# Optimization experiments

Measured on AMD Instinct MI355X. Metric: run time of the kernel, lower is better.

## Reference

```python
import jax, jax.numpy as jnp
import numpy as np

N, E, B, A = 102400, 1638400, 256, 7


def setup_inputs() -> dict:
    key = jax.random.key(0)
    ks = jax.random.split(key, 24)
    rn = lambda k, s, sc=0.1: jax.random.normal(k, s, jnp.float32) * sc
    return {
        "x": jax.random.normal(ks[0], (N, 5), jnp.float32),
        "edge_index": jax.random.randint(ks[1], (2, E), 0, N, jnp.int32),
        "edge_attr": jax.random.normal(ks[2], (E, 1), jnp.float32),
        "agent_state": jax.random.normal(ks[3], (B, 34), jnp.float32),
        "pool_batch": jnp.sort(jax.random.randint(ks[4], (N,), 0, B, jnp.int32)),
        # GATConv params (heads=1, concat): lin [5,64], lin_edge [1,64], att vectors [64], bias [64]
        "W_gat": rn(ks[5], (5, 64)), "att_src": rn(ks[6], (64,)), "att_dst": rn(ks[7], (64,)),
        "W_edge": rn(ks[8], (1, 64)), "att_edge": rn(ks[9], (64,)), "b_gat": rn(ks[10], (64,)),
        "W_fc1": rn(ks[11], (64, 128)), "b_fc1": rn(ks[12], (128,)),
        "W_fc2": rn(ks[13], (34, 64)), "b_fc2": rn(ks[14], (64,)),
        "W_v1": rn(ks[15], (192, 128)), "b_v1": rn(ks[16], (128,)),
        "W_v2": rn(ks[17], (128, 1)), "b_v2": rn(ks[18], (1,)),
        "W_a1": rn(ks[19], (192, 128)), "b_a1": rn(ks[20], (128,)),
        "W_a2": rn(ks[21], (128, A)), "b_a2": rn(ks[22], (A,)),
    }


def _gat(x, edge_index, edge_attr, W_gat, att_src, att_dst, W_edge, att_edge, b_gat):
    n = x.shape[0]
    # add self-loops (PyG default), self-loop edge_attr = mean of edge_attr
    loop = jnp.arange(n, dtype=edge_index.dtype)
    src = jnp.concatenate([edge_index[0], loop])
    dst = jnp.concatenate([edge_index[1], loop])
    ea = jnp.concatenate([edge_attr, jnp.broadcast_to(edge_attr.mean(0), (n, edge_attr.shape[1]))], 0)
    h = x @ W_gat                                  # [N,64]
    a_s = h @ att_src                              # [N]
    a_d = h @ att_dst                              # [N]
    a_e = (ea @ W_edge) @ att_edge                 # [E+N]
    alpha = jax.nn.leaky_relu(a_s[src] + a_d[dst] + a_e, 0.2)
    # segment softmax over incoming edges per destination node
    m = jax.ops.segment_max(alpha, dst, num_segments=n)
    ex = jnp.exp(alpha - m[dst])
    s = jax.ops.segment_sum(ex, dst, num_segments=n)
    w = ex / (s[dst] + 1e-16)
    out = jax.ops.segment_sum(w[:, None] * h[src], dst, num_segments=n)
    return out + b_gat


def reference(x, edge_index, edge_attr, agent_state, pool_batch,
              W_gat, att_src, att_dst, W_edge, att_edge, b_gat,
              W_fc1, b_fc1, W_fc2, b_fc2,
              W_v1, b_v1, W_v2, b_v2, W_a1, b_a1, W_a2, b_a2):
    h = _gat(x, edge_index, edge_attr, W_gat, att_src, att_dst, W_edge, att_edge, b_gat)
    h = jax.nn.relu(h @ W_fc1 + b_fc1)             # [N,128]
    # global mean pool over graphs
    ssum = jax.ops.segment_sum(h, pool_batch, num_segments=B)
    cnt = jax.ops.segment_sum(jnp.ones((h.shape[0],), h.dtype), pool_batch, num_segments=B)
    g = ssum / jnp.maximum(cnt, 1.0)[:, None]      # [B,128]
    a = jax.nn.relu(agent_state @ W_fc2 + b_fc2)   # [B,64]
    z = jnp.concatenate([g, a], -1)                # [B,192]
    value = jax.nn.relu(z @ W_v1 + b_v1) @ W_v2 + b_v2
    adv = jax.nn.relu(z @ W_a1 + b_a1) @ W_a2 + b_a2
    return value + adv - adv.mean(-1, keepdims=True)
```

## Files before the change

kernel.cpp:

```cpp
#include <hip/hip_runtime.h>
#include <hip/hip_fp16.h>
#include <math.h>

#define NPB   512
#define NPBL  9
#define HSTR  5
#define MAXR  256
#define TILE  2048
#define RPT   8
#define GCS   16
#define SLICES 8

static __device__ __forceinline__ float lrelu(float x) { return x > 0.0f ? x : 0.2f * x; }

static __device__ __forceinline__ unsigned pk2(float a, float b) {
    __half2 h = __floats2half2_rn(a, b);
    return *reinterpret_cast<unsigned*>(&h);
}
static __device__ __forceinline__ float2 up2(unsigned u) {
    __half2 h = *reinterpret_cast<__half2*>(&u);
    return __half22float2(h);
}


__global__ void k_setup(const float* __restrict__ W_gat, const float* __restrict__ att_src,
                        const float* __restrict__ att_dst, const float* __restrict__ W_edge,
                        const float* __restrict__ att_edge, const float* __restrict__ b_gat,
                        const float* __restrict__ W_fc1, const float* __restrict__ b_fc1,
                        float* __restrict__ consts, unsigned* __restrict__ gcur,
                        float* __restrict__ epart8) {
    int t = threadIdx.x;
    for (int i = t; i < MAXR * GCS; i += 128) gcur[i] = 0u;
    if (t < 8) epart8[t] = 0.f;
    if (t == 0) {
        float c = 0.f;
        for (int k = 0; k < 64; k++) c += W_edge[k] * att_edge[k];
        consts[1] = c;
    }
    if (t < 5) {
        float a = 0.f, b = 0.f;
        for (int c = 0; c < 64; c++) {
            float w = W_gat[t * 64 + c];
            a += w * att_src[c];
            b += w * att_dst[c];
        }
        consts[2 + t] = a;
        consts[7 + t] = b;
    }
    float bcv = b_fc1[t];
    for (int c = 0; c < 64; c++) bcv += b_gat[c] * W_fc1[c * 128 + t];
    consts[16 + t] = bcv;
    for (int k = 0; k < 5; k++) {
        float w = 0.f;
        for (int c = 0; c < 64; c++) w += W_gat[k * 64 + c] * W_fc1[c * 128 + t];
        consts[144 + k * 128 + t] = w;
    }
}

__global__ void k_np1(const float* __restrict__ x, const float* __restrict__ consts,
                      uint4* __restrict__ xh, float* __restrict__ a_s, float* __restrict__ a_d,
                      const int* __restrict__ pb, int* __restrict__ bstart,
                      const int* __restrict__ src, const int* __restrict__ dst,
                      const float* __restrict__ ea,
                      uint2* __restrict__ slab, unsigned* __restrict__ gcur,
                      float* __restrict__ epart8,
                      int N, int B, int E, int R, int CAP, int nbl) {
    if ((int)blockIdx.x < nbl) {
        int i = blockIdx.x * blockDim.x + threadIdx.x;
        if (i >= N) return;
        const float* xi = x + (size_t)i * 5;
        float x0 = xi[0], x1 = xi[1], x2 = xi[2], x3 = xi[3], x4 = xi[4];
        float as = x0 * consts[2] + x1 * consts[3] + x2 * consts[4] + x3 * consts[5] + x4 * consts[6];
        float ad = x0 * consts[7] + x1 * consts[8] + x2 * consts[9] + x3 * consts[10] + x4 * consts[11];
        uint4 pkv;
        pkv.x = pk2(x0, x1);
        pkv.y = pk2(x2, x3);
        pkv.z = pk2(x4, 1.0f);
        pkv.w = __float_as_uint(as);
        xh[i] = pkv;
        a_s[i] = as;
        a_d[i] = ad;
        int cur = pb[i];
        int prev = (i == 0) ? -1 : pb[i - 1];
        for (int b = prev + 1; b <= cur; b++) bstart[b] = i;
        if (i == N - 1)
            for (int b = cur + 1; b <= B; b++) bstart[b] = N;
        return;
    }
    __shared__ unsigned hist[MAXR], lbase[MAXR], gbase[MAXR], scan[256];
    __shared__ uint2 staged[TILE];
    __shared__ unsigned char bof[TILE];
    __shared__ float esum[256];
    int t = threadIdx.x;
    int e0 = ((int)blockIdx.x - nbl) * TILE;
    int n = E - e0; if (n > TILE) n = TILE;
    for (int i = t; i < MAXR; i += 256) hist[i] = 0;
    __syncthreads();
    unsigned key[RPT]; float val[RPT]; unsigned brk[RPT];
    float ce = consts[1];
    float easc = 0.f;
#pragma unroll
    for (int k = 0; k < RPT; k++) {
        int idx = t + k * 256;
        brk[k] = 0xFFFFFFFFu;
        if (idx < n) {
            int e = e0 + idx;
            int d = dst[e];
            unsigned b = (unsigned)d >> NPBL;
            key[k] = ((unsigned)src[e] << NPBL) | ((unsigned)d & (NPB - 1));
            float eav = ea[e];
            easc += eav;
            val[k] = ce * eav;
            unsigned r = atomicAdd(&hist[b], 1u);
            brk[k] = (b << 12) | r;
        }
    }
    __syncthreads();
    unsigned v = (t < R) ? hist[t] : 0;
    if (t < R) gbase[t] = atomicAdd(&gcur[t * GCS], v);
    scan[t] = v;
    __syncthreads();
    for (int off = 1; off < 256; off <<= 1) {
        unsigned add = (t >= off) ? scan[t - off] : 0;
        __syncthreads();
        scan[t] += add;
        __syncthreads();
    }
    if (t < R) lbase[t] = scan[t] - v;
    __syncthreads();
#pragma unroll
    for (int k = 0; k < RPT; k++) {
        if (brk[k] != 0xFFFFFFFFu) {
            unsigned b = brk[k] >> 12, r = brk[k] & 4095u;
            unsigned pos = lbase[b] + r;
            staged[pos] = make_uint2(key[k], __float_as_uint(val[k]));
            bof[pos] = (unsigned char)b;
        }
    }
    __syncthreads();
    for (int i = t; i < n; i += 256) {
        unsigned b = bof[i];
        unsigned slot = gbase[b] + (unsigned)i - lbase[b];
        if (slot < (unsigned)CAP) slab[(size_t)b * CAP + slot] = staged[i];
    }
    esum[t] = easc;
    __syncthreads();
    for (int o = 128; o > 0; o >>= 1) {
        if (t < o) esum[t] += esum[t + o];
        __syncthreads();
    }
    if (t == 0) unsafeAtomicAdd(&epart8[blockIdx.x & 7], esum[0]);
}

__global__ void k_p2(const uint2* __restrict__ slab, const unsigned* __restrict__ gcur,
                     const uint4* __restrict__ xh, const float* __restrict__ a_d,
                     unsigned* __restrict__ partials, const float* __restrict__ epart8,
                     float* __restrict__ consts_w, int S, int CAP, int N) {
    __shared__ __half2 accH[NPB * HSTR];
    __shared__ float adl[NPB];
    int t = threadIdx.x;
    int s = blockIdx.x, r = blockIdx.y;
    if (s == 0 && r == 0 && t == 0) {
        float se = 0.f;
        for (int i = 0; i < 8; i++) se += epart8[i];
        consts_w[0] = se;
    }
    for (int i = t; i < NPB; i += 256) {
        int node = r * NPB + i;
        adl[i] = (node < N) ? a_d[node] : 0.f;
    }
    __half2 z2 = __floats2half2_rn(0.f, 0.f);
    for (int i = t; i < NPB * HSTR; i += 256) accH[i] = z2;
    __syncthreads();
    unsigned cnt = gcur[r * GCS]; if (cnt > (unsigned)CAP) cnt = CAP;
    unsigned L = (cnt + (unsigned)S - 1) / (unsigned)S;
    unsigned i0 = (unsigned)s * L, i1 = i0 + L; if (i1 > cnt) i1 = cnt;
    const uint2* sl = slab + (size_t)r * CAP;
    for (unsigned i = i0 + t; i < i1; i += 256) {
        uint2 rec = sl[i];
        uint4 v = xh[rec.x >> NPBL];
        unsigned dl = rec.x & (NPB - 1);
        float al = __uint_as_float(v.w) + adl[dl] + __uint_as_float(rec.y);
        float ex = __expf(lrelu(al));
        __half2 ex2 = __half2half2(__float2half(ex));
        __half2* a = accH + dl * HSTR;
        unsafeAtomicAdd(a + 0, __hmul2(ex2, *reinterpret_cast<const __half2*>(&v.x)));
        unsafeAtomicAdd(a + 1, __hmul2(ex2, *reinterpret_cast<const __half2*>(&v.y)));
        unsafeAtomicAdd(a + 2, __hmul2(ex2, *reinterpret_cast<const __half2*>(&v.z)));
    }
    __syncthreads();
    unsigned* out = partials + (size_t)(r * S + s) * (NPB * 3);
    for (int j = t; j < NPB * 3; j += 256) {
        int comp = j >> NPBL, dl = j & (NPB - 1);
        out[j] = *reinterpret_cast<unsigned*>(&accH[dl * HSTR + comp]);
    }
}

__global__ void k_p3(const unsigned* __restrict__ partials, const float* __restrict__ x,
                     const float* __restrict__ a_s, const float* __restrict__ a_d,
                     const float* __restrict__ consts, float* __restrict__ y,
                     int N, int S, float inv_E) {
    int i = blockIdx.x * blockDim.x + threadIdx.x;
    if (i >= N) return;
    int r = i >> NPBL, dl = i & (NPB - 1);
    float2 y01 = make_float2(0.f, 0.f), y23 = make_float2(0.f, 0.f), y4s = make_float2(0.f, 0.f);
    const unsigned* p = partials + (size_t)r * S * (NPB * 3) + dl;
    for (int s = 0; s < S; s++) {
        const unsigned* q = p + (size_t)s * (NPB * 3);
        float2 a = up2(q[0 * NPB]), b = up2(q[1 * NPB]), c = up2(q[2 * NPB]);
        y01.x += a.x; y01.y += a.y;
        y23.x += b.x; y23.y += b.y;
        y4s.x += c.x; y4s.y += c.y;
    }
    const float* xi = x + (size_t)i * 5;
    float x0 = xi[0], x1 = xi[1], x2 = xi[2], x3 = xi[3], x4 = xi[4];
    float mean_ea = consts[0] * inv_E;
    float aself = lrelu(a_s[i] + a_d[i] + consts[1] * mean_ea);
    float exs = __expf(aself);
    float inv = 1.f / (y4s.y + exs + 1e-16f);
    y[0 * (size_t)N + i] = (y01.x + exs * x0) * inv;
    y[1 * (size_t)N + i] = (y01.y + exs * x1) * inv;
    y[2 * (size_t)N + i] = (y23.x + exs * x2) * inv;
    y[3 * (size_t)N + i] = (y23.y + exs * x3) * inv;
    y[4 * (size_t)N + i] = (y4s.x + exs * x4) * inv;
}

__global__ void k_pool(const float* __restrict__ y, const float* __restrict__ consts,
                       const int* __restrict__ bstart, float* __restrict__ g4, int B, int N) {
    int l = threadIdx.x;
    int b = blockIdx.x >> 2, q = blockIdx.x & 3;
    int st = bstart[b], en = bstart[b + 1];
    int len = en - st;
    int qlen = (len + 3) >> 2;
    int i0 = st + q * qlen;
    int i1 = i0 + qlen;
    if (i0 > en) i0 = en;
    if (i1 > en) i1 = en;
    float w0 = consts[144 + l], w1 = consts[272 + l], w2 = consts[400 + l],
          w3 = consts[528 + l], w4 = consts[656 + l];
    float bc = consts[16 + l];
    const float* y0 = y;
    const float* y1p = y + (size_t)N;
    const float* y2p = y + 2 * (size_t)N;
    const float* y3p = y + 3 * (size_t)N;
    const float* y4p = y + 4 * (size_t)N;
    float a0 = 0.f, a1 = 0.f, a2 = 0.f, a3 = 0.f;
    int i = i0;
    for (; i + 3 < i1; i += 4) {
        float h0 = bc + y0[i] * w0 + y1p[i] * w1 + y2p[i] * w2 + y3p[i] * w3 + y4p[i] * w4;
        float h1 = bc + y0[i+1] * w0 + y1p[i+1] * w1 + y2p[i+1] * w2 + y3p[i+1] * w3 + y4p[i+1] * w4;
        float h2 = bc + y0[i+2] * w0 + y1p[i+2] * w1 + y2p[i+2] * w2 + y3p[i+2] * w3 + y4p[i+2] * w4;
        float h3 = bc + y0[i+3] * w0 + y1p[i+3] * w1 + y2p[i+3] * w2 + y3p[i+3] * w3 + y4p[i+3] * w4;
        a0 += fmaxf(h0, 0.f);
        a1 += fmaxf(h1, 0.f);
        a2 += fmaxf(h2, 0.f);
        a3 += fmaxf(h3, 0.f);
    }
    for (; i < i1; ++i) {
        float h = bc + y0[i] * w0 + y1p[i] * w1 + y2p[i] * w2 + y3p[i] * w3 + y4p[i] * w4;
        a0 += fmaxf(h, 0.f);
    }
    g4[((size_t)q * B + b) * 128 + l] = (a0 + a1) + (a2 + a3);
}

__global__ void k_head(const float* __restrict__ g4, const int* __restrict__ bstart,
                       const float* __restrict__ agent_state, const float* __restrict__ W_fc2,
                       const float* __restrict__ b_fc2, const float* __restrict__ W_v1,
                       const float* __restrict__ b_v1, const float* __restrict__ W_v2,
                       const float* __restrict__ b_v2, const float* __restrict__ W_a1,
                       const float* __restrict__ b_a1, const float* __restrict__ W_a2,
                       const float* __restrict__ b_a2, float* __restrict__ out, int A, int B) {
    __shared__ float z[192];
    __shared__ float part[4][128];
    __shared__ float va[256];
    __shared__ float red[128];
    __shared__ float advs[8];
    int b = blockIdx.x, t = threadIdx.x;
    int col = t & 127, grp = t >> 7;
    if (t < 128) {
        float cnt = (float)(bstart[b + 1] - bstart[b]);
        cnt = cnt < 1.f ? 1.f : cnt;
        z[t] = (g4[(size_t)b * 128 + t] + g4[((size_t)B + b) * 128 + t]
              + g4[(2 * (size_t)B + b) * 128 + t] + g4[(3 * (size_t)B + b) * 128 + t]) / cnt;
    } else if (t < 192) {
        int c = t - 128;
        float a = b_fc2[c];
        const float* as_ = agent_state + b * 34;
        for (int k = 0; k < 34; k++) a += as_[k] * W_fc2[k * 64 + c];
        z[128 + c] = fmaxf(a, 0.f);
    }
    __syncthreads();
    {
        const float* W = (grp & 2) ? W_a1 : W_v1;
        int j0 = (grp & 1) * 96;
        float c0 = 0.f, c1 = 0.f, c2 = 0.f, c3 = 0.f;
        for (int j = j0; j < j0 + 96; j += 4) {
            c0 += z[j]     * W[(size_t)j * 128 + col];
            c1 += z[j + 1] * W[(size_t)(j + 1) * 128 + col];
            c2 += z[j + 2] * W[(size_t)(j + 2) * 128 + col];
            c3 += z[j + 3] * W[(size_t)(j + 3) * 128 + col];
        }
        part[grp][col] = (c0 + c1) + (c2 + c3);
    }
    __syncthreads();
    if (t < 128) {
        float v = fmaxf(b_v1[t] + part[0][t] + part[1][t], 0.f);
        va[t] = v;
        red[t] = v * W_v2[t];
    } else if (t < 256) {
        va[t] = fmaxf(b_a1[col] + part[2][col] + part[3][col], 0.f);
    }
    __syncthreads();
    for (int o = 64; o > 0; o >>= 1) {
        if (t < o) red[t] += red[t + o];
        __syncthreads();
    }
    if (t < A * 64) {
        int oc = t >> 6, lane = t & 63;
        float s = va[128 + lane] * W_a2[(size_t)lane * A + oc]
                + va[128 + 64 + lane] * W_a2[(size_t)(64 + lane) * A + oc];
        for (int o = 32; o > 0; o >>= 1) s += __shfl_down(s, o, 64);
        if (lane == 0) advs[oc] = s + b_a2[oc];
    }
    __syncthreads();
    if (t == 0) {
        float value = red[0] + b_v2[0];
        float m = 0.f;
        for (int j = 0; j < A; j++) m += advs[j];
        m *= (1.f / (float)A);
        for (int j = 0; j < A; j++) out[b * A + j] = value + advs[j] - m;
    }
}

extern "C" void kernel_launch(void* const* d_in, const int* in_sizes, int n_in,
                              void* d_out, int out_size, void* d_ws, size_t ws_size,
                              hipStream_t stream) {
    const float* x        = (const float*)d_in[0];
    const int* edge_index = (const int*)d_in[1];
    const float* ea       = (const float*)d_in[2];
    const float* agent    = (const float*)d_in[3];
    const int* pool_batch = (const int*)d_in[4];
    const float* W_gat    = (const float*)d_in[5];
    const float* att_src  = (const float*)d_in[6];
    const float* att_dst  = (const float*)d_in[7];
    const float* W_edge   = (const float*)d_in[8];
    const float* att_edge = (const float*)d_in[9];
    const float* b_gat    = (const float*)d_in[10];
    const float* W_fc1    = (const float*)d_in[11];
    const float* b_fc1    = (const float*)d_in[12];
    const float* W_fc2    = (const float*)d_in[13];
    const float* b_fc2    = (const float*)d_in[14];
    const float* W_v1     = (const float*)d_in[15];
    const float* b_v1     = (const float*)d_in[16];
    const float* W_v2     = (const float*)d_in[17];
    const float* b_v2     = (const float*)d_in[18];
    const float* W_a1     = (const float*)d_in[19];
    const float* b_a1     = (const float*)d_in[20];
    const float* W_a2     = (const float*)d_in[21];
    const float* b_a2     = (const float*)d_in[22];

    const int N = in_sizes[0] / 5;
    const int E = in_sizes[2];
    const int B = in_sizes[3] / 34;
    const int A = out_size / B;
    const float inv_E = 1.0f / (float)E;

    const int* src = edge_index;
    const int* dst = edge_index + E;

    const int R = (N + NPB - 1) / NPB;
    int capBase = (E + R - 1) / R;
    const int CAP = capBase + capBase / 16 + 256;

    char* ws = (char*)d_ws;
    size_t off = 0;
    auto take = [&](size_t bytes) {
        size_t o = off;
        off = (off + bytes + 255) & ~(size_t)255;
        return o;
    };
    size_t o_consts = take(4096);
    size_t o_gcur   = take((size_t)MAXR * GCS * 4);
    size_t o_epart8 = take(8 * 4);
    size_t o_xh     = take((size_t)N * 16);
    size_t o_as     = take((size_t)N * 4);
    size_t o_ad     = take((size_t)N * 4);
    size_t o_y      = take((size_t)N * 5 * 4);
    size_t o_bstart = take((size_t)(B + 1) * 4);
    size_t o_g4     = take((size_t)4 * B * 128 * 4);
    size_t o_slab   = take((size_t)R * CAP * 8);
    size_t o_part   = off;
    size_t perS = (size_t)R * NPB * 3 * 4;
    int S = SLICES;
    while (S > 1 && o_part + (size_t)S * perS > ws_size) S--;

    float* consts   = (float*)(ws + o_consts);
    unsigned* gcur  = (unsigned*)(ws + o_gcur);
    float* epart8   = (float*)(ws + o_epart8);
    uint4* xh       = (uint4*)(ws + o_xh);
    float* a_s      = (float*)(ws + o_as);
    float* a_d      = (float*)(ws + o_ad);
    float* y        = (float*)(ws + o_y);
    int* bstart     = (int*)(ws + o_bstart);
    float* g4       = (float*)(ws + o_g4);
    uint2* slab     = (uint2*)(ws + o_slab);
    unsigned* partials = (unsigned*)(ws + o_part);

    k_setup<<<1, 128, 0, stream>>>(W_gat, att_src, att_dst, W_edge, att_edge, b_gat,
                                   W_fc1, b_fc1, consts, gcur, epart8);

    int nbl = (N + 255) / 256;
    int ebl = (E + TILE - 1) / TILE;
    k_np1<<<nbl + ebl, 256, 0, stream>>>(x, consts, xh, a_s, a_d, pool_batch, bstart,
                                         src, dst, ea, slab, gcur, epart8,
                                         N, B, E, R, CAP, nbl);
    dim3 g2grid(S, R);
    k_p2<<<g2grid, 256, 0, stream>>>(slab, gcur, xh, a_d, partials, epart8, consts, S, CAP, N);
    k_p3<<<nbl, 256, 0, stream>>>(partials, x, a_s, a_d, consts, y, N, S, inv_E);
    k_pool<<<4 * B, 128, 0, stream>>>(y, consts, bstart, g4, B, N);
    k_head<<<B, 512, 0, stream>>>(g4, bstart, agent, W_fc2, b_fc2, W_v1, b_v1, W_v2, b_v2,
                                  W_a1, b_a1, W_a2, b_a2, (float*)d_out, A, B);
}
```

Baseline: 106.5 us.

## Fuse partial reduction into scatter kernel via last-block counter; merge pool and head

```diff
diff --git a/kernel.cpp b/kernel.cpp
--- a/kernel.cpp
+++ b/kernel.cpp
@@ -28,9 +28,9 @@
                         const float* __restrict__ att_edge, const float* __restrict__ b_gat,
                         const float* __restrict__ W_fc1, const float* __restrict__ b_fc1,
                         float* __restrict__ consts, unsigned* __restrict__ gcur,
-                        float* __restrict__ epart8) {
+                        unsigned* __restrict__ rdone, float* __restrict__ epart8) {
     int t = threadIdx.x;
-    for (int i = t; i < MAXR * GCS; i += 128) gcur[i] = 0u;
+    for (int i = t; i < MAXR * GCS; i += 128) { gcur[i] = 0u; rdone[i] = 0u; }
     if (t < 8) epart8[t] = 0.f;
     if (t == 0) {
         float c = 0.f;
@@ -155,16 +155,15 @@
 __global__ void k_p2(const uint2* __restrict__ slab, const unsigned* __restrict__ gcur,
                      const uint4* __restrict__ xh, const float* __restrict__ a_d,
                      unsigned* __restrict__ partials, const float* __restrict__ epart8,
-                     float* __restrict__ consts_w, int S, int CAP, int N) {
+                     unsigned* __restrict__ rdone,
+                     const float* __restrict__ x, const float* __restrict__ a_s,
+                     const float* __restrict__ consts, float* __restrict__ y,
+                     int S, int CAP, int N, float inv_E) {
     __shared__ __half2 accH[NPB * HSTR];
     __shared__ float adl[NPB];
+    __shared__ unsigned lastflag;
     int t = threadIdx.x;
     int s = blockIdx.x, r = blockIdx.y;
-    if (s == 0 && r == 0 && t == 0) {
-        float se = 0.f;
-        for (int i = 0; i < 8; i++) se += epart8[i];
-        consts_w[0] = se;
-    }
     for (int i = t; i < NPB; i += 256) {
         int node = r * NPB + i;
         adl[i] = (node < N) ? a_d[node] : 0.f;
@@ -194,94 +193,99 @@
         int comp = j >> NPBL, dl = j & (NPB - 1);
         out[j] = *reinterpret_cast<unsigned*>(&accH[dl * HSTR + comp]);
     }
-}
-
-__global__ void k_p3(const unsigned* __restrict__ partials, const float* __restrict__ x,
-                     const float* __restrict__ a_s, const float* __restrict__ a_d,
-                     const float* __restrict__ consts, float* __restrict__ y,
-                     int N, int S, float inv_E) {
-    int i = blockIdx.x * blockDim.x + threadIdx.x;
-    if (i >= N) return;
-    int r = i >> NPBL, dl = i & (NPB - 1);
-    float2 y01 = make_float2(0.f, 0.f), y23 = make_float2(0.f, 0.f), y4s = make_float2(0.f, 0.f);
-    const unsigned* p = partials + (size_t)r * S * (NPB * 3) + dl;
-    for (int s = 0; s < S; s++) {
-        const unsigned* q = p + (size_t)s * (NPB * 3);
-        float2 a = up2(q[0 * NPB]), b = up2(q[1 * NPB]), c = up2(q[2 * NPB]);
-        y01.x += a.x; y01.y += a.y;
-        y23.x += b.x; y23.y += b.y;
-        y4s.x += c.x; y4s.y += c.y;
-    }
-    const float* xi = x + (size_t)i * 5;
-    float x0 = xi[0], x1 = xi[1], x2 = xi[2], x3 = xi[3], x4 = xi[4];
-    float mean_ea = consts[0] * inv_E;
-    float aself = lrelu(a_s[i] + a_d[i] + consts[1] * mean_ea);
-    float exs = __expf(aself);
-    float inv = 1.f / (y4s.y + exs + 1e-16f);
-    y[0 * (size_t)N + i] = (y01.x + exs * x0) * inv;
-    y[1 * (size_t)N + i] = (y01.y + exs * x1) * inv;
-    y[2 * (size_t)N + i] = (y23.x + exs * x2) * inv;
-    y[3 * (size_t)N + i] = (y23.y + exs * x3) * inv;
-    y[4 * (size_t)N + i] = (y4s.x + exs * x4) * inv;
-}
-
-__global__ void k_pool(const float* __restrict__ y, const float* __restrict__ consts,
-                       const int* __restrict__ bstart, float* __restrict__ g4, int B, int N) {
-    int l = threadIdx.x;
-    int b = blockIdx.x >> 2, q = blockIdx.x & 3;
-    int st = bstart[b], en = bstart[b + 1];
-    int len = en - st;
-    int qlen = (len + 3) >> 2;
-    int i0 = st + q * qlen;
-    int i1 = i0 + qlen;
-    if (i0 > en) i0 = en;
-    if (i1 > en) i1 = en;
-    float w0 = consts[144 + l], w1 = consts[272 + l], w2 = consts[400 + l],
-          w3 = consts[528 + l], w4 = consts[656 + l];
-    float bc = consts[16 + l];
-    const float* y0 = y;
-    const float* y1p = y + (size_t)N;
-    const float* y2p = y + 2 * (size_t)N;
-    const float* y3p = y + 3 * (size_t)N;
-    const float* y4p = y + 4 * (size_t)N;
-    float a0 = 0.f, a1 = 0.f, a2 = 0.f, a3 = 0.f;
-    int i = i0;
-    for (; i + 3 < i1; i += 4) {
-        float h0 = bc + y0[i] * w0 + y1p[i] * w1 + y2p[i] * w2 + y3p[i] * w3 + y4p[i] * w4;
-        float h1 = bc + y0[i+1] * w0 + y1p[i+1] * w1 + y2p[i+1] * w2 + y3p[i+1] * w3 + y4p[i+1] * w4;
-        float h2 = bc + y0[i+2] * w0 + y1p[i+2] * w1 + y2p[i+2] * w2 + y3p[i+2] * w3 + y4p[i+2] * w4;
-        float h3 = bc + y0[i+3] * w0 + y1p[i+3] * w1 + y2p[i+3] * w2 + y3p[i+3] * w3 + y4p[i+3] * w4;
-        a0 += fmaxf(h0, 0.f);
-        a1 += fmaxf(h1, 0.f);
-        a2 += fmaxf(h2, 0.f);
-        a3 += fmaxf(h3, 0.f);
-    }
-    for (; i < i1; ++i) {
-        float h = bc + y0[i] * w0 + y1p[i] * w1 + y2p[i] * w2 + y3p[i] * w3 + y4p[i] * w4;
-        a0 += fmaxf(h, 0.f);
-    }
-    g4[((size_t)q * B + b) * 128 + l] = (a0 + a1) + (a2 + a3);
-}
-
-__global__ void k_head(const float* __restrict__ g4, const int* __restrict__ bstart,
-                       const float* __restrict__ agent_state, const float* __restrict__ W_fc2,
-                       const float* __restrict__ b_fc2, const float* __restrict__ W_v1,
-                       const float* __restrict__ b_v1, const float* __restrict__ W_v2,
-                       const float* __restrict__ b_v2, const float* __restrict__ W_a1,
-                       const float* __restrict__ b_a1, const float* __restrict__ W_a2,
-                       const float* __restrict__ b_a2, float* __restrict__ out, int A, int B) {
+    __syncthreads();
+    if (t == 0) {
+        __threadfence();
+        unsigned prev = atomicAdd(&rdone[r * GCS], 1u);
+        lastflag = (prev == (unsigned)(S - 1)) ? 1u : 0u;
+    }
+    __syncthreads();
+    if (!lastflag) return;
+    __threadfence();
+    float se = 0.f;
+    for (int k2 = 0; k2 < 8; k2++) se += epart8[k2];
+    float mean_ea = se * inv_E;
+    float cedge = consts[1];
+    for (int dl = t; dl < NPB; dl += 256) {
+        int i = r * NPB + dl;
+        if (i >= N) break;
+        float2 y01 = make_float2(0.f, 0.f), y23 = make_float2(0.f, 0.f), y4s = make_float2(0.f, 0.f);
+        const unsigned* p = partials + (size_t)r * S * (NPB * 3) + dl;
+        for (int s2 = 0; s2 < S; s2++) {
+            const unsigned* q = p + (size_t)s2 * (NPB * 3);
+            float2 a = up2(q[0 * NPB]), bv = up2(q[1 * NPB]), c = up2(q[2 * NPB]);
+            y01.x += a.x; y01.y += a.y;
+            y23.x += bv.x; y23.y += bv.y;
+            y4s.x += c.x; y4s.y += c.y;
+        }
+        const float* xi = x + (size_t)i * 5;
+        float x0 = xi[0], x1 = xi[1], x2 = xi[2], x3 = xi[3], x4 = xi[4];
+        float aself = lrelu(a_s[i] + adl[dl] + cedge * mean_ea);
+        float exs = __expf(aself);
+        float inv = 1.f / (y4s.y + exs + 1e-16f);
+        y[0 * (size_t)N + i] = (y01.x + exs * x0) * inv;
+        y[1 * (size_t)N + i] = (y01.y + exs * x1) * inv;
+        y[2 * (size_t)N + i] = (y23.x + exs * x2) * inv;
+        y[3 * (size_t)N + i] = (y23.y + exs * x3) * inv;
+        y[4 * (size_t)N + i] = (y4s.x + exs * x4) * inv;
+    }
+}
+
+__global__ void k_poolhead(const float* __restrict__ y, const float* __restrict__ consts,
+                           const int* __restrict__ bstart, const float* __restrict__ agent_state,
+                           const float* __restrict__ W_fc2, const float* __restrict__ b_fc2,
+                           const float* __restrict__ W_v1, const float* __restrict__ b_v1,
+                           const float* __restrict__ W_v2, const float* __restrict__ b_v2,
+                           const float* __restrict__ W_a1, const float* __restrict__ b_a1,
+                           const float* __restrict__ W_a2, const float* __restrict__ b_a2,
+                           float* __restrict__ out, int A, int B, int N) {
+    __shared__ float part[4][128];
+    __shared__ float gpart[4][128];
     __shared__ float z[192];
-    __shared__ float part[4][128];
     __shared__ float va[256];
     __shared__ float red[128];
     __shared__ float advs[8];
     int b = blockIdx.x, t = threadIdx.x;
     int col = t & 127, grp = t >> 7;
+    int st = bstart[b], en = bstart[b + 1];
+    int len = en - st;
+    {
+        int qlen = (len + 3) >> 2;
+        int i0 = st + grp * qlen;
+        int i1 = i0 + qlen;
+        if (i0 > en) i0 = en;
+        if (i1 > en) i1 = en;
+        float w0 = consts[144 + col], w1 = consts[272 + col], w2 = consts[400 + col],
+              w3 = consts[528 + col], w4 = consts[656 + col];
+        float bc = consts[16 + col];
+        const float* y0 = y;
+        const float* y1p = y + (size_t)N;
+        const float* y2p = y + 2 * (size_t)N;
+        const float* y3p = y + 3 * (size_t)N;
+        const float* y4p = y + 4 * (size_t)N;
+        float a0 = 0.f, a1 = 0.f, a2 = 0.f, a3 = 0.f;
+        int i = i0;
+        for (; i + 3 < i1; i += 4) {
+            float h0 = bc + y0[i] * w0 + y1p[i] * w1 + y2p[i] * w2 + y3p[i] * w3 + y4p[i] * w4;
+            float h1 = bc + y0[i+1] * w0 + y1p[i+1] * w1 + y2p[i+1] * w2 + y3p[i+1] * w3 + y4p[i+1] * w4;
+            float h2 = bc + y0[i+2] * w0 + y1p[i+2] * w1 + y2p[i+2] * w2 + y3p[i+2] * w3 + y4p[i+2] * w4;
+            float h3 = bc + y0[i+3] * w0 + y1p[i+3] * w1 + y2p[i+3] * w2 + y3p[i+3] * w3 + y4p[i+3] * w4;
+            a0 += fmaxf(h0, 0.f);
+            a1 += fmaxf(h1, 0.f);
+            a2 += fmaxf(h2, 0.f);
+            a3 += fmaxf(h3, 0.f);
+        }
+        for (; i < i1; ++i) {
+            float h = bc + y0[i] * w0 + y1p[i] * w1 + y2p[i] * w2 + y3p[i] * w3 + y4p[i] * w4;
+            a0 += fmaxf(h, 0.f);
+        }
+        part[grp][col] = (a0 + a1) + (a2 + a3);
+    }
+    __syncthreads();
     if (t < 128) {
-        float cnt = (float)(bstart[b + 1] - bstart[b]);
+        float cnt = (float)len;
         cnt = cnt < 1.f ? 1.f : cnt;
-        z[t] = (g4[(size_t)b * 128 + t] + g4[((size_t)B + b) * 128 + t]
-              + g4[(2 * (size_t)B + b) * 128 + t] + g4[(3 * (size_t)B + b) * 128 + t]) / cnt;
+        z[t] = (part[0][t] + part[1][t] + part[2][t] + part[3][t]) / cnt;
     } else if (t < 192) {
         int c = t - 128;
         float a = b_fc2[c];
@@ -300,15 +304,15 @@
             c2 += z[j + 2] * W[(size_t)(j + 2) * 128 + col];
             c3 += z[j + 3] * W[(size_t)(j + 3) * 128 + col];
         }
-        part[grp][col] = (c0 + c1) + (c2 + c3);
+        gpart[grp][col] = (c0 + c1) + (c2 + c3);
     }
     __syncthreads();
     if (t < 128) {
-        float v = fmaxf(b_v1[t] + part[0][t] + part[1][t], 0.f);
+        float v = fmaxf(b_v1[t] + gpart[0][t] + gpart[1][t], 0.f);
         va[t] = v;
         red[t] = v * W_v2[t];
     } else if (t < 256) {
-        va[t] = fmaxf(b_a1[col] + part[2][col] + part[3][col], 0.f);
+        va[t] = fmaxf(b_a1[col] + gpart[2][col] + gpart[3][col], 0.f);
     }
     __syncthreads();
     for (int o = 64; o > 0; o >>= 1) {
@@ -381,13 +385,13 @@
     };
     size_t o_consts = take(4096);
     size_t o_gcur   = take((size_t)MAXR * GCS * 4);
+    size_t o_rdone  = take((size_t)MAXR * GCS * 4);
     size_t o_epart8 = take(8 * 4);
     size_t o_xh     = take((size_t)N * 16);
     size_t o_as     = take((size_t)N * 4);
     size_t o_ad     = take((size_t)N * 4);
     size_t o_y      = take((size_t)N * 5 * 4);
     size_t o_bstart = take((size_t)(B + 1) * 4);
-    size_t o_g4     = take((size_t)4 * B * 128 * 4);
     size_t o_slab   = take((size_t)R * CAP * 8);
     size_t o_part   = off;
     size_t perS = (size_t)R * NPB * 3 * 4;
@@ -396,18 +400,18 @@
 
     float* consts   = (float*)(ws + o_consts);
     unsigned* gcur  = (unsigned*)(ws + o_gcur);
+    unsigned* rdone = (unsigned*)(ws + o_rdone);
     float* epart8   = (float*)(ws + o_epart8);
     uint4* xh       = (uint4*)(ws + o_xh);
     float* a_s      = (float*)(ws + o_as);
     float* a_d      = (float*)(ws + o_ad);
     float* y        = (float*)(ws + o_y);
     int* bstart     = (int*)(ws + o_bstart);
-    float* g4       = (float*)(ws + o_g4);
     uint2* slab     = (uint2*)(ws + o_slab);
     unsigned* partials = (unsigned*)(ws + o_part);
 
     k_setup<<<1, 128, 0, stream>>>(W_gat, att_src, att_dst, W_edge, att_edge, b_gat,
-                                   W_fc1, b_fc1, consts, gcur, epart8);
+                                   W_fc1, b_fc1, consts, gcur, rdone, epart8);
 
     int nbl = (N + 255) / 256;
     int ebl = (E + TILE - 1) / TILE;
@@ -415,9 +419,9 @@
                                          src, dst, ea, slab, gcur, epart8,
                                          N, B, E, R, CAP, nbl);
     dim3 g2grid(S, R);
-    k_p2<<<g2grid, 256, 0, stream>>>(slab, gcur, xh, a_d, partials, epart8, consts, S, CAP, N);
-    k_p3<<<nbl, 256, 0, stream>>>(partials, x, a_s, a_d, consts, y, N, S, inv_E);
-    k_pool<<<4 * B, 128, 0, stream>>>(y, consts, bstart, g4, B, N);
-    k_head<<<B, 512, 0, stream>>>(g4, bstart, agent, W_fc2, b_fc2, W_v1, b_v1, W_v2, b_v2,
-                                  W_a1, b_a1, W_a2, b_a2, (float*)d_out, A, B);
-}
+    k_p2<<<g2grid, 256, 0, stream>>>(slab, gcur, xh, a_d, partials, epart8, rdone,
+                                     x, a_s, consts, y, S, CAP, N, inv_E);
+    k_poolhead<<<B, 512, 0, stream>>>(y, consts, bstart, agent, W_fc2, b_fc2,
+                                      W_v1, b_v1, W_v2, b_v2, W_a1, b_a1, W_a2, b_a2,
+                                      (float*)d_out, A, B, N);
+}
```

After: 210.8 us. 98.0% more time.
